# Kernel tuning notes

Hardware: AMD Instinct MI355X
Metric: run time of the kernel (lower is better)

## Reference

```python
import jax, jax.numpy as jnp
import numpy as np

TEMPERATURE = 0.1
NUM_CLASSES = 100


def setup_inputs() -> dict:
    key = jax.random.key(0)
    k1, k2 = jax.random.split(key)
    embeddings = jax.random.normal(k1, (8192, 128), dtype=jnp.float32)
    labels = jax.random.randint(k2, (8192,), 0, NUM_CLASSES, dtype=jnp.int64)
    return {"embeddings": embeddings, "labels": labels}


def reference(embeddings, labels):
    # L2-normalize rows (eps matches torch.nn.functional.normalize clamp)
    norm = jnp.maximum(jnp.linalg.norm(embeddings, axis=1, keepdims=True), 1e-12)
    e = embeddings / norm
    sim = jnp.matmul(e, e.T) / TEMPERATURE  # [N, N]
    n = sim.shape[0]
    eye = jnp.eye(n, dtype=bool)
    # positives: same label, excluding self
    pos = (labels[None, :] == labels[:, None]) & ~eye
    # The per-row torch loop computes soft-target cross-entropy over all
    # non-diagonal entries: row_loss_i = -sum_{j in pos(i)} log_softmax(sim[i, j!=i])_j.
    # log_softmax is permutation-invariant, so concatenation order is irrelevant.
    neg_inf = jnp.finfo(sim.dtype).min
    masked = jnp.where(eye, neg_inf, sim)
    logz = jax.nn.logsumexp(masked, axis=1, keepdims=True)  # [N, 1]
    logp = sim - logz  # [N, N]
    row_loss = -jnp.sum(jnp.where(pos, logp, 0.0), axis=1)  # rows with no positives contribute 0
    return jnp.sum(row_loss) / n
```

## Files before the change

kernel.cpp:

```cpp
#include <hip/hip_runtime.h>


#define N 8192
#define D 128
#define NCLS 100
#define NTILE 512
#define RLCAP 256
#define IBLK 256
#define MWIN 8
#define YGRID 32
#define LDS_TILES 20
#define K2E 14.4269504088896340736f
#define LN2 0.69314718055994530942f

typedef __bf16 bf16x8 __attribute__((ext_vector_type(8)));
typedef float f32x4 __attribute__((ext_vector_type(4)));

#define EBF_OFF  0x000000u
#define ENORM_OFF 0x200000u
#define CNT_OFF  0x600000u
#define Z_OFF    0x600200u
#define RL_OFF   0x608200u
#define S_OFF    0x621200u
#define ZERO_SZ  (512u + 32768u)

__device__ __forceinline__ unsigned short f32_to_bf16_rne(float f) {
    unsigned int u = __float_as_uint(f);
    u += 0x7fffu + ((u >> 16) & 1u);
    return (unsigned short)(u >> 16);
}


__global__ __launch_bounds__(256) void prep_kernel(
        const float* __restrict__ emb, const int* __restrict__ labels,
        unsigned char* __restrict__ ebf, int* __restrict__ cnt,
        float* __restrict__ enorm, int* __restrict__ rowlist) {
    const int wave = threadIdx.x >> 6;
    const int lane = threadIdx.x & 63;
    const int row  = blockIdx.x * 4 + wave;

    const float2 v = *(const float2*)(emb + (size_t)row * D + lane * 2);
    float ss = v.x * v.x + v.y * v.y;
    #pragma unroll
    for (int off = 32; off; off >>= 1) ss += __shfl_xor(ss, off);
    const float inv = 1.0f / fmaxf(sqrtf(ss), 1e-12f);
    const float ex = v.x * inv, ey = v.y * inv;

    const int grp = row >> 4, col = row & 15;
    const int c = lane >> 4, q = (lane >> 2) & 3, j2 = lane & 3;
    unsigned int packed = (unsigned int)f32_to_bf16_rne(ex) |
                          ((unsigned int)f32_to_bf16_rne(ey) << 16);
    *(unsigned int*)(ebf + grp * 4096 + c * 1024 + q * 256 + col * 16 + j2 * 4) = packed;

    float2* ep = (float2*)(enorm + (size_t)row * D + lane * 2);
    *ep = make_float2(ex, ey);

    if (lane == 0) {
        const int lab = labels[row];
        int slot = atomicAdd(&cnt[lab], 1);
        slot = slot < RLCAP ? slot : RLCAP - 1;
        rowlist[lab * RLCAP + slot] = row;
    }
}

__global__ __launch_bounds__(128) void classsum_kernel(
        const float* __restrict__ enorm, const int* __restrict__ cnt,
        const int* __restrict__ rowlist, float* __restrict__ S) {
    const int c = blockIdx.x;
    const int d = threadIdx.x;
    const int n = cnt[c] < RLCAP ? cnt[c] : RLCAP;
    const int* rl = rowlist + c * RLCAP;
    float acc = 0.0f;
    int idx = 0;
    for (; idx + 4 <= n; idx += 4) {
        const int r0 = rl[idx], r1 = rl[idx + 1], r2 = rl[idx + 2], r3 = rl[idx + 3];
        acc += enorm[(size_t)r0 * D + d] + enorm[(size_t)r1 * D + d]
             + enorm[(size_t)r2 * D + d] + enorm[(size_t)r3 * D + d];
    }
    for (; idx < n; ++idx)
        acc += enorm[(size_t)rl[idx] * D + d];
    S[c * D + d] = acc;
}

__global__ __launch_bounds__(256) void zsum_kernel(
        const unsigned char* __restrict__ ebf, float* __restrict__ z) {
    __shared__ float zcol[LDS_TILES * 16];
    const int t    = threadIdx.x;
    const int w    = t >> 6;
    const int lane = t & 63;
    const int q    = lane >> 4;
    const int col  = lane & 15;
    const int bi   = blockIdx.x;
    const int y    = blockIdx.y;
    const int ti0  = bi * 16 + w * 4;
    const int m_lo = y * MWIN + 1;
    const bool lowhalf = (bi < 16);

    for (int e = t; e < LDS_TILES * 16; e += 256) zcol[e] = 0.0f;

    bf16x8 a[4][4];
    #pragma unroll
    for (int g = 0; g < 4; ++g) {
        const unsigned char* ag = ebf + (size_t)(ti0 + g) * 4096 + lane * 16;
        #pragma unroll
        for (int c = 0; c < 4; ++c) a[g][c] = *(const bf16x8*)(ag + c * 1024);
    }

    float zacc[4][4] = {{0.f,0.f,0.f,0.f},{0.f,0.f,0.f,0.f},
                        {0.f,0.f,0.f,0.f},{0.f,0.f,0.f,0.f}};

    __syncthreads();

    if (y == 0) {
        #pragma unroll
        for (int g = 0; g < 4; ++g) {
            const unsigned char* bg = ebf + (size_t)(ti0 + g) * 4096 + lane * 16;
            bf16x8 bd[4];
            #pragma unroll
            for (int c = 0; c < 4; ++c) bd[c] = *(const bf16x8*)(bg + c * 1024);
            f32x4 acc = {0.f, 0.f, 0.f, 0.f};
            #pragma unroll
            for (int c = 0; c < 4; ++c)
                acc = __builtin_amdgcn_mfma_f32_16x16x32_bf16(a[g][c], bd[c], acc, 0, 0, 0);
            #pragma unroll
            for (int r = 0; r < 4; ++r)
                zacc[g][r] += (col == q * 4 + r) ? 0.0f
                    : __builtin_amdgcn_exp2f(fmaf(acc[r], K2E, -K2E));
        }
    }

    const int ns = MWIN + ((y == 29 || y == 30 || (y == 31 && lowhalf)) ? 1 : 0);
    const int m_x = 228 + y;

    bf16x8 bc[4];
    {
        const int tj = (ti0 + m_lo) & (NTILE - 1);
        const unsigned char* bg = ebf + (size_t)tj * 4096 + lane * 16;
        #pragma unroll
        for (int c = 0; c < 4; ++c) bc[c] = *(const bf16x8*)(bg + c * 1024);
    }

    #pragma unroll 2
    for (int s = 0; s < ns; ++s) {
        const int m = (s < MWIN) ? (m_lo + s) : m_x;

        const int sn = (s + 1 < ns) ? s + 1 : s;
        const int mn = (sn < MWIN) ? (m_lo + sn) : m_x;
        bf16x8 bn[4];
        {
            const int tjn = (ti0 + mn) & (NTILE - 1);
            const unsigned char* bg = ebf + (size_t)tjn * 4096 + lane * 16;
            #pragma unroll
            for (int c = 0; c < 4; ++c) bn[c] = *(const bf16x8*)(bg + c * 1024);
        }

        float ctot = 0.0f;
        #pragma unroll
        for (int g = 0; g < 4; ++g) {
            const int d = m - g;
            const bool act = (d >= 1 && d <= 255) || (d == 256 && lowhalf);
            if (act) {
                f32x4 acc = {0.f, 0.f, 0.f, 0.f};
                __builtin_amdgcn_s_setprio(1);
                #pragma unroll
                for (int c = 0; c < 4; ++c)
                    acc = __builtin_amdgcn_mfma_f32_16x16x32_bf16(a[g][c], bc[c], acc, 0, 0, 0);
                __builtin_amdgcn_s_setprio(0);
                #pragma unroll
                for (int r = 0; r < 4; ++r) {
                    const float p = __builtin_amdgcn_exp2f(fmaf(acc[r], K2E, -K2E));
                    zacc[g][r] += p;
                    ctot += p;
                }
            }
        }

        ctot += __shfl_xor(ctot, 16);
        ctot += __shfl_xor(ctot, 32);
        if (q == 0 && ctot != 0.0f) {
            if (s < MWIN) {
                const int rel = w * 4 + (m - m_lo);
                atomicAdd(&zcol[rel * 16 + col], ctot);
            } else {
                const int tj = (ti0 + m) & (NTILE - 1);
                atomicAdd(&z[tj * 16 + col], ctot);
            }
        }

        #pragma unroll
        for (int c = 0; c < 4; ++c) bc[c] = bn[c];
    }

    #pragma unroll
    for (int g = 0; g < 4; ++g)
        #pragma unroll
        for (int r = 0; r < 4; ++r) {
            float zv = zacc[g][r];
            zv += __shfl_xor(zv, 1);
            zv += __shfl_xor(zv, 2);
            zv += __shfl_xor(zv, 4);
            zv += __shfl_xor(zv, 8);
            if (col == 0)
                atomicAdd(&z[(ti0 + g) * 16 + q * 4 + r], zv);
        }

    __syncthreads();
    for (int e = t; e < LDS_TILES * 16; e += 256) {
        const float v = zcol[e];
        if (v != 0.0f) {
            const int tj = (bi * 16 + m_lo + (e >> 4)) & (NTILE - 1);
            atomicAdd(&z[tj * 16 + (e & 15)], v);
        }
    }
}

__global__ __launch_bounds__(1024) void final_kernel(
        const int* __restrict__ labels, const int* __restrict__ cnt,
        const float* __restrict__ z, const float* __restrict__ S,
        float* __restrict__ out) {
    __shared__ float part[16];
    const int tid = threadIdx.x;
    float acc = 0.0f;
    #pragma unroll
    for (int k = 0; k < N / 1024; ++k) {
        const int row = k * 1024 + tid;
        const int P = cnt[labels[row]] - 1;
        if (P > 0)
            acc += (float)P * fmaf(LN2, __builtin_amdgcn_logf(z[row]), 10.0f);
    }
    #pragma unroll
    for (int k = 0; k < (NCLS * D + 1023) / 1024; ++k) {
        const int idx = k * 1024 + tid;
        if (idx < NCLS * D) {
            const float sv = S[idx];
            acc -= 10.0f * sv * sv;
        }
    }
    #pragma unroll
    for (int off = 32; off; off >>= 1) acc += __shfl_xor(acc, off);
    if ((tid & 63) == 0) part[tid >> 6] = acc;
    __syncthreads();
    if (tid == 0) {
        float tot = 0.0f;
        #pragma unroll
        for (int w = 0; w < 16; ++w) tot += part[w];
        out[0] = (tot + 10.0f * (float)N) * (1.0f / (float)N);
    }
}

extern "C" void kernel_launch(void* const* d_in, const int* in_sizes, int n_in,
                              void* d_out, int out_size, void* d_ws, size_t ws_size,
                              hipStream_t stream) {
    const float* emb  = (const float*)d_in[0];
    const int* labels = (const int*)d_in[1];
    float* out        = (float*)d_out;
    char* ws          = (char*)d_ws;

    unsigned char* ebf = (unsigned char*)(ws + EBF_OFF);
    float* enorm       = (float*)(ws + ENORM_OFF);
    int*   cnt         = (int*)(ws + CNT_OFF);
    float* z           = (float*)(ws + Z_OFF);
    int*   rowlist     = (int*)(ws + RL_OFF);
    float* S           = (float*)(ws + S_OFF);

    hipMemsetAsync(ws + CNT_OFF, 0, ZERO_SZ, stream);

    prep_kernel<<<N / 4, 256, 0, stream>>>(emb, labels, ebf, cnt, enorm, rowlist);
    classsum_kernel<<<NCLS, 128, 0, stream>>>(enorm, cnt, rowlist, S);
    zsum_kernel<<<dim3(N / IBLK, YGRID), 256, 0, stream>>>(ebf, z);
    final_kernel<<<1, 1024, 0, stream>>>(labels, cnt, z, S, out);
}
```

Before: 125.1 us.

## Fuse class-sum into zsum grid and widen prep loads to float4

The class-sum kernel becomes extra blocks (x>=32) of the zsum launch, so per-class feature sums run alongside the similarity tiles and one kernel launch and its dependency gap go away. The prep kernel now handles two rows per wave with float4 loads and 8-byte bf16 stores, halving its block count. The extra blocks could shift scheduling of the main zsum work, and most of them only use half their threads.

```diff
diff --git a/kernel.cpp b/kernel.cpp
--- a/kernel.cpp
+++ b/kernel.cpp
@@ -6,9 +6,9 @@
 #define NCLS 100
 #define NTILE 512
 #define RLCAP 256
-#define IBLK 256
 #define MWIN 8
 #define YGRID 32
+#define XGRID 36
 #define LDS_TILES 20
 #define K2E 14.4269504088896340736f
 #define LN2 0.69314718055994530942f
@@ -35,27 +35,29 @@
         const float* __restrict__ emb, const int* __restrict__ labels,
         unsigned char* __restrict__ ebf, int* __restrict__ cnt,
         float* __restrict__ enorm, int* __restrict__ rowlist) {
-    const int wave = threadIdx.x >> 6;
+    const int w    = threadIdx.x >> 6;
     const int lane = threadIdx.x & 63;
-    const int row  = blockIdx.x * 4 + wave;
-
-    const float2 v = *(const float2*)(emb + (size_t)row * D + lane * 2);
-    float ss = v.x * v.x + v.y * v.y;
-    #pragma unroll
-    for (int off = 32; off; off >>= 1) ss += __shfl_xor(ss, off);
+    const int h    = lane >> 5;
+    const int li   = lane & 31;
+    const int row  = blockIdx.x * 8 + w * 2 + h;
+
+    const float4 v = *(const float4*)(emb + (size_t)row * D + li * 4);
+    float ss = v.x * v.x + v.y * v.y + v.z * v.z + v.w * v.w;
+    #pragma unroll
+    for (int off = 16; off; off >>= 1) ss += __shfl_xor(ss, off);
     const float inv = 1.0f / fmaxf(sqrtf(ss), 1e-12f);
-    const float ex = v.x * inv, ey = v.y * inv;
+    const float e0 = v.x * inv, e1 = v.y * inv, e2 = v.z * inv, e3 = v.w * inv;
 
     const int grp = row >> 4, col = row & 15;
-    const int c = lane >> 4, q = (lane >> 2) & 3, j2 = lane & 3;
-    unsigned int packed = (unsigned int)f32_to_bf16_rne(ex) |
-                          ((unsigned int)f32_to_bf16_rne(ey) << 16);
-    *(unsigned int*)(ebf + grp * 4096 + c * 1024 + q * 256 + col * 16 + j2 * 4) = packed;
-
-    float2* ep = (float2*)(enorm + (size_t)row * D + lane * 2);
-    *ep = make_float2(ex, ey);
-
-    if (lane == 0) {
+    const int c = li >> 3, q = (li >> 1) & 3, jh = li & 1;
+    uint2 packed;
+    packed.x = (unsigned)f32_to_bf16_rne(e0) | ((unsigned)f32_to_bf16_rne(e1) << 16);
+    packed.y = (unsigned)f32_to_bf16_rne(e2) | ((unsigned)f32_to_bf16_rne(e3) << 16);
+    *(uint2*)(ebf + grp * 4096 + c * 1024 + q * 256 + col * 16 + jh * 8) = packed;
+
+    *(float4*)(enorm + (size_t)row * D + li * 4) = make_float4(e0, e1, e2, e3);
+
+    if (li == 0) {
         const int lab = labels[row];
         int slot = atomicAdd(&cnt[lab], 1);
         slot = slot < RLCAP ? slot : RLCAP - 1;
@@ -63,29 +65,32 @@
     }
 }
 
-__global__ __launch_bounds__(128) void classsum_kernel(
+__global__ __launch_bounds__(256) void zsum_kernel(
+        const unsigned char* __restrict__ ebf, float* __restrict__ z,
         const float* __restrict__ enorm, const int* __restrict__ cnt,
         const int* __restrict__ rowlist, float* __restrict__ S) {
-    const int c = blockIdx.x;
-    const int d = threadIdx.x;
-    const int n = cnt[c] < RLCAP ? cnt[c] : RLCAP;
-    const int* rl = rowlist + c * RLCAP;
-    float acc = 0.0f;
-    int idx = 0;
-    for (; idx + 4 <= n; idx += 4) {
-        const int r0 = rl[idx], r1 = rl[idx + 1], r2 = rl[idx + 2], r3 = rl[idx + 3];
-        acc += enorm[(size_t)r0 * D + d] + enorm[(size_t)r1 * D + d]
-             + enorm[(size_t)r2 * D + d] + enorm[(size_t)r3 * D + d];
-    }
-    for (; idx < n; ++idx)
-        acc += enorm[(size_t)rl[idx] * D + d];
-    S[c * D + d] = acc;
-}
-
-__global__ __launch_bounds__(256) void zsum_kernel(
-        const unsigned char* __restrict__ ebf, float* __restrict__ z) {
+    const int t = threadIdx.x;
+
+    if (blockIdx.x >= 32) {
+        const int eidx = (blockIdx.x - 32) * YGRID + blockIdx.y;
+        if (eidx >= NCLS || t >= 128) return;
+        const int d = t;
+        const int n = cnt[eidx] < RLCAP ? cnt[eidx] : RLCAP;
+        const int* rl = rowlist + eidx * RLCAP;
+        float acc = 0.0f;
+        int idx = 0;
+        for (; idx + 4 <= n; idx += 4) {
+            const int r0 = rl[idx], r1 = rl[idx + 1], r2 = rl[idx + 2], r3 = rl[idx + 3];
+            acc += enorm[(size_t)r0 * D + d] + enorm[(size_t)r1 * D + d]
+                 + enorm[(size_t)r2 * D + d] + enorm[(size_t)r3 * D + d];
+        }
+        for (; idx < n; ++idx)
+            acc += enorm[(size_t)rl[idx] * D + d];
+        S[eidx * D + d] = acc;
+        return;
+    }
+
     __shared__ float zcol[LDS_TILES * 16];
-    const int t    = threadIdx.x;
     const int w    = t >> 6;
     const int lane = t & 63;
     const int q    = lane >> 4;
@@ -265,8 +270,7 @@
 
     hipMemsetAsync(ws + CNT_OFF, 0, ZERO_SZ, stream);
 
-    prep_kernel<<<N / 4, 256, 0, stream>>>(emb, labels, ebf, cnt, enorm, rowlist);
-    classsum_kernel<<<NCLS, 128, 0, stream>>>(enorm, cnt, rowlist, S);
-    zsum_kernel<<<dim3(N / IBLK, YGRID), 256, 0, stream>>>(ebf, z);
+    prep_kernel<<<N / 8, 256, 0, stream>>>(emb, labels, ebf, cnt, enorm, rowlist);
+    zsum_kernel<<<dim3(XGRID, YGRID), 256, 0, stream>>>(ebf, z, enorm, cnt, rowlist, S);
     final_kernel<<<1, 1024, 0, stream>>>(labels, cnt, z, S, out);
 }
```

Measured after the change: 115.9 us. -7.4%, faster.
